# Optimization experiments

Hardware: AMD Instinct MI355X
Metric: run time of the kernel (lower is better)

The kernel has to match this reference:

```python
import jax, jax.numpy as jnp
import numpy as np

N = 1536          # num nodes
E = 49152         # num edges (avg degree 32)
D_IN = 32         # in_channels_node
D_EA = 2          # in_channels_edge_attr
D_ET = 2          # in_channels_edge_type
EMB = 32          # edge_attr_emb = edge_type_emb = node_emb = out_channels
HEADS = 3
SLOPE = 0.2


def leaky(x):
    return jax.nn.leaky_relu(x, negative_slope=SLOPE)


def setup_inputs() -> dict:
    key = jax.random.key(0)
    ks = jax.random.split(key, 12)
    node_f = jax.random.normal(ks[0], (N, D_IN), dtype=jnp.float32)
    edge_index = jax.random.randint(ks[1], (2, E), 0, N, dtype=jnp.int32)
    edge_attr = jax.random.normal(ks[2], (E, D_EA), dtype=jnp.float32)
    edge_type = jax.random.uniform(ks[3], (E, D_ET), dtype=jnp.float32)
    veh_node_mask = jax.random.bernoulli(ks[4], 0.7, (N,))
    ped_node_mask = jnp.logical_not(veh_node_mask)
    s = 0.1
    W_veh = jax.random.normal(ks[5], (EMB, D_IN), dtype=jnp.float32) * s
    W_ped = jax.random.normal(ks[6], (EMB, D_IN), dtype=jnp.float32) * s
    W_ea = jax.random.normal(ks[7], (EMB, D_EA), dtype=jnp.float32) * s
    W_et = jax.random.normal(ks[8], (EMB, D_ET), dtype=jnp.float32) * s
    # attention_nn: Linear(edge_attr_emb + edge_type_emb + 2*node_emb -> heads)
    W_att = jax.random.normal(ks[9], (HEADS, 2 * EMB + 2 * EMB), dtype=jnp.float32) * s
    # node_update_emb: Linear(edge_attr_emb + node_emb -> out_channels)
    W_upd = jax.random.normal(ks[10], (EMB, 2 * EMB), dtype=jnp.float32) * s
    return dict(node_f=node_f, edge_attr=edge_attr, edge_type=edge_type,
                W_veh=W_veh, W_ped=W_ped, W_ea=W_ea, W_et=W_et,
                W_att=W_att, W_upd=W_upd,
                edge_index=edge_index, veh_node_mask=veh_node_mask,
                ped_node_mask=ped_node_mask)


def reference(node_f, edge_attr, edge_type, W_veh, W_ped, W_ea, W_et,
              W_att, W_upd, edge_index, veh_node_mask, ped_node_mask):
    n = node_f.shape[0]
    src, dst = edge_index[0], edge_index[1]

    # edge embeddings [E, 32] each
    emb_ea = leaky(edge_attr @ W_ea.T)
    emb_et = leaky(edge_type.astype(node_f.dtype) @ W_et.T)
    edge_f = jnp.concatenate([emb_ea, emb_et], axis=-1)        # [E, 64]

    # densify (sparse_coo_tensor -> to_dense sums duplicate indices)
    dense_edge = jnp.zeros((n, n, 2 * EMB), node_f.dtype).at[src, dst].add(edge_f)
    dense_ea = jnp.zeros((n, n, EMB), node_f.dtype).at[src, dst].add(emb_ea)
    adj = jnp.zeros((n, n), node_f.dtype).at[src, dst].add(1.0)

    # type-specific node embedding (ped assignment last, matching torch overwrite order)
    node_emb = jnp.where(veh_node_mask[:, None], node_f @ W_veh.T, 0.0)
    node_emb = jnp.where(ped_node_mask[:, None], node_f @ W_ped.T, node_emb)
    node_emb = leaky(node_emb)                                  # [N, 32]

    # attention scores: split the linear over the concatenated [tar | edge | nbr] features
    W_tar, W_edge, W_nbr = W_att[:, :EMB], W_att[:, EMB:3 * EMB], W_att[:, 3 * EMB:]
    scores = leaky((node_emb @ W_tar.T)[:, None, :]
                   + jnp.einsum('ijc,hc->ijh', dense_edge, W_edge)
                   + (node_emb @ W_nbr.T)[None, :, :])          # [N, N, H]

    scores = jnp.where(adj[:, :, None] == 0.0, jnp.float32(-10000.0), scores)
    attn = jax.nn.softmax(scores, axis=1)                       # softmax over neighbors

    # node update features: Linear over [edge_attr_emb | nbr_emb]; identical across heads
    Wu_e, Wu_n = W_upd[:, :EMB], W_upd[:, EMB:]
    upd = leaky(jnp.einsum('ijc,oc->ijo', dense_ea, Wu_e)
                + (node_emb @ Wu_n.T)[None, :, :])              # [N, N, 32]

    # weighted aggregation over neighbors, then concat heads
    next_node_f = jnp.einsum('ijh,ijo->iho', attn, upd)         # [N, H, 32]
    return next_node_f.reshape(n, HEADS * EMB)
```

## Files before the change

### kernel.cpp

```cpp
#include <hip/hip_runtime.h>
#include <stdint.h>

#define NN 1536
#define EE 49152
#define EMB 32
#define HEADS 3
#define SLOPE 0.2f
#define CAP 72
#define EBLK (EE/256)
#define NBLK (NN/8)

__device__ __forceinline__ float lrelu(float x){ return x >= 0.f ? x : SLOPE*x; }

__device__ int detect_mask_layout(const unsigned char* p){
  const int* pi = (const int*)p;
  bool ok = true;
  for (int k=0;k<64 && ok;k++){ int v = pi[k]; ok = (v==0 || v==1); }
  if (ok) return 0;
  ok = true;
  for (int k=0;k<256 && ok;k++){ ok = (p[k] <= 1); }
  if (ok) return 1;
  return 2;
}
__device__ bool mask_at(const unsigned char* p, int layout, int i){
  if (layout==0) return ((const int*)p)[i] != 0;
  if (layout==1) return p[i] != 0;
  return ((const float*)p)[i] != 0.f;
}

__global__ __launch_bounds__(256) void k_prep(
    const float* __restrict__ node_f,
    const float* __restrict__ edge_attr, const float* __restrict__ edge_type,
    const float* __restrict__ W_veh, const float* __restrict__ W_ped,
    const float* __restrict__ W_att, const float* __restrict__ W_upd,
    const int* __restrict__ ei, const unsigned char* __restrict__ veh_mask,
    int* __restrict__ cnt, int* __restrict__ bucketD, float4* __restrict__ bucketF,
    float* __restrict__ tar, float* __restrict__ nbr, float* __restrict__ nb)
{
  const int t = threadIdx.x;
  const int b = blockIdx.x;

  if (b < EBLK){
    const int e = b*256 + t;
    const int s = ei[e], d = ei[EE + e];
    const float2 ea = ((const float2*)edge_attr)[e];
    const float2 et = ((const float2*)edge_type)[e];
    const int idx = atomicAdd(&cnt[s], 1);
    if (idx < CAP){
      bucketD[(size_t)s*CAP + idx] = d;
      bucketF[(size_t)s*CAP + idx] = make_float4(ea.x, ea.y, et.x, et.y);
    }
    return;
  }

  __shared__ float sWvehT[EMB*33], sWpedT[EMB*33], sWunT[EMB*33];
  __shared__ float sWt[HEADS*EMB], sWn[HEADS*EMB];
  __shared__ float sF[8*EMB], sEmb[8*EMB];
  __shared__ int layout_s;
  const int i0 = (b - EBLK)*8;
  if (t == 0) layout_s = detect_mask_layout(veh_mask);
  for (int idx=t; idx<EMB*EMB; idx+=256){
    const int mm = idx>>5, kk = idx&31;
    sWvehT[mm*33+kk] = W_veh[idx];
    sWpedT[mm*33+kk] = W_ped[idx];
    sWunT[mm*33+kk]  = W_upd[mm*64 + EMB + kk];
  }
  if (t < HEADS*EMB){
    const int h = t>>5, c = t&31;
    sWt[t] = W_att[h*128 + c];
    sWn[t] = W_att[h*128 + 96 + c];
  }
  sF[t] = node_f[(size_t)i0*EMB + t];
  __syncthreads();

  const int li = t >> 5, m = t & 31;
  const int i = i0 + li;
  const bool veh = mask_at(veh_mask, layout_s, i);
  const float* WT = veh ? sWvehT : sWpedT;
  float a = 0.f;
  #pragma unroll
  for (int k=0;k<EMB;k++) a += sF[li*EMB+k] * WT[m*33+k];
  sEmb[li*EMB+m] = lrelu(a);
  __syncthreads();

  float bb = 0.f;
  #pragma unroll
  for (int k=0;k<EMB;k++) bb += sEmb[li*EMB+k] * sWunT[m*33+k];
  nb[(size_t)i*EMB + m] = bb;
  if (m < 3){
    float v = 0.f;
    #pragma unroll
    for (int k=0;k<EMB;k++) v += sEmb[li*EMB+k] * sWt[m*EMB+k];
    tar[i*4+m] = v;
  } else if (m < 6){
    const int h = m-3;
    float v = 0.f;
    #pragma unroll
    for (int k=0;k<EMB;k++) v += sEmb[li*EMB+k] * sWn[h*EMB+k];
    nbr[i*4+h] = v;
  }
}

__global__ __launch_bounds__(256) void k_rows(
    const int* __restrict__ cnt, const int* __restrict__ bucketD,
    const float4* __restrict__ bucketF,
    const float* __restrict__ W_ea, const float* __restrict__ W_et,
    const float* __restrict__ W_att, const float* __restrict__ W_upd,
    const float* __restrict__ tar, const float* __restrict__ nbr,
    const float* __restrict__ nb, float* __restrict__ out)
{
  const int r = blockIdx.x;
  const int t = threadIdx.x;

  __shared__ int   ld[CAP], canon[CAP], slotidx[CAP], slotof[CAP], cdst[CAP];
  __shared__ float4 pay[CAP];
  __shared__ float sE[CAP*66];
  __shared__ float sWea[64], sWet[64], sWedge[HEADS*64], sWueT[EMB*33];
  __shared__ float pp[HEADS*CAP];
  __shared__ float partial[8*96];
  __shared__ float hden[HEADS];
  __shared__ int np_s;

  if (t < 64){ sWea[t] = W_ea[t]; sWet[t] = W_et[t]; }
  if (t < HEADS*64) sWedge[t] = W_att[(t>>6)*128 + EMB + (t&63)];
  for (int idx=t; idx<EMB*EMB; idx+=256){
    const int o = idx>>5, k = idx&31;
    sWueT[o*33+k] = W_upd[o*64 + k];
  }
  if (t == 0) np_s = 0;

  const int K = min(cnt[r], CAP);

  if (K == 0){
    __shared__ float fb[EMB];
    if (t < EMB) fb[t] = 0.f;
    __syncthreads();
    for (int idx=t; idx<NN*EMB; idx+=256) atomicAdd(&fb[idx&31], lrelu(nb[idx]));
    __syncthreads();
    if (t < 96) out[(size_t)r*96 + t] = fb[t&31] * (1.0f/NN);
    return;
  }

  for (int i=t; i<K; i+=256){
    ld[i]  = bucketD[(size_t)r*CAP + i];
    pay[i] = bucketF[(size_t)r*CAP + i];
    canon[i] = i;
  }
  __syncthreads();

  for (int p=t; p<K*K; p+=256){
    const int i = p / K, j = p - i*K;
    if (j < i && ld[i] == ld[j]) atomicMin(&canon[i], j);
  }
  __syncthreads();
  for (int i=t; i<K; i+=256){
    if (canon[i] == i){
      const int s2 = atomicAdd(&np_s, 1);
      slotidx[i] = s2;
      cdst[s2]   = ld[i];
    }
  }
  __syncthreads();
  const int Kc = np_s;
  const bool nodup = (Kc == K);

  for (int i=t; i<K; i+=256) slotof[i] = slotidx[canon[i]];
  if (!nodup){
    for (int idx=t; idx<Kc*66; idx+=256) sE[idx] = 0.f;
  }
  __syncthreads();

  for (int idx=t; idx<K*EMB; idx+=256){
    const int q = idx>>5, m = idx&31;
    const float4 p4 = pay[q];
    const float ea_ = lrelu(p4.x*sWea[2*m] + p4.y*sWea[2*m+1]);
    const float et_ = lrelu(p4.z*sWet[2*m] + p4.w*sWet[2*m+1]);
    const int sl = slotof[q];
    if (nodup){
      sE[sl*66 + m]      = ea_;
      sE[sl*66 + 33 + m] = et_;
    } else {
      atomicAdd(&sE[sl*66 + m],      ea_);
      atomicAdd(&sE[sl*66 + 33 + m], et_);
    }
  }
  __syncthreads();

  if (t < 192){
    const int h = t >> 6, lane = t & 63;
    const float th = tar[r*4+h];
    float mx = -1e30f;
    for (int q0=0; q0<Kc; q0+=64){
      const int q = q0 + lane;
      if (q < Kc){
        float sev = 0.f;
        #pragma unroll
        for (int k=0;k<EMB;k++)
          sev += sWedge[h*64+k]*sE[q*66+k] + sWedge[h*64+EMB+k]*sE[q*66+33+k];
        const float s = lrelu(th + sev + nbr[cdst[q]*4+h]);
        pp[h*CAP+q] = s;
        mx = fmaxf(mx, s);
      }
    }
    #pragma unroll
    for (int d=32; d; d>>=1) mx = fmaxf(mx, __shfl_xor(mx, d, 64));
    float den = 0.f;
    for (int q0=0; q0<Kc; q0+=64){
      const int q = q0 + lane;
      if (q < Kc){
        const float p = __expf(pp[h*CAP+q] - mx);
        pp[h*CAP+q] = p;
        den += p;
      }
    }
    #pragma unroll
    for (int d=32; d; d>>=1) den += __shfl_xor(den, d, 64);
    if (lane == 0) hden[h] = den;
  }
  __syncthreads();

  {
    const int g = t >> 5, o = t & 31;
    float a0=0.f, a1=0.f, a2=0.f;
    for (int q=g; q<Kc; q+=8){
      float ev = 0.f;
      #pragma unroll
      for (int k=0;k<EMB;k++) ev += sWueT[o*33+k] * sE[q*66+k];
      const float u = lrelu(ev + nb[(size_t)cdst[q]*EMB + o]);
      a0 += pp[0*CAP+q]*u;
      a1 += pp[1*CAP+q]*u;
      a2 += pp[2*CAP+q]*u;
    }
    partial[g*96 +      o] = a0;
    partial[g*96 + 32 + o] = a1;
    partial[g*96 + 64 + o] = a2;
  }
  __syncthreads();
  if (t < 96){
    float s = 0.f;
    #pragma unroll
    for (int g=0; g<8; g++) s += partial[g*96 + t];
    out[(size_t)r*96 + t] = s / hden[t>>5];
  }
}

extern "C" void kernel_launch(void* const* d_in, const int* in_sizes, int n_in,
                              void* d_out, int out_size, void* d_ws, size_t ws_size,
                              hipStream_t stream)
{
  (void)in_sizes; (void)n_in; (void)out_size; (void)ws_size;
  const float* node_f    = (const float*)d_in[0];
  const float* edge_attr = (const float*)d_in[1];
  const float* edge_type = (const float*)d_in[2];
  const float* W_veh     = (const float*)d_in[3];
  const float* W_ped     = (const float*)d_in[4];
  const float* W_ea      = (const float*)d_in[5];
  const float* W_et      = (const float*)d_in[6];
  const float* W_att     = (const float*)d_in[7];
  const float* W_upd     = (const float*)d_in[8];
  const int*   ei        = (const int*)d_in[9];
  const unsigned char* veh_mask = (const unsigned char*)d_in[10];
  float* out = (float*)d_out;

  char* ws = (char*)d_ws;
  const size_t oCnt  = 0;
  const size_t oBktF = oCnt  + (size_t)NN*4;
  const size_t oBktD = oBktF + (size_t)NN*CAP*16;
  const size_t oTar  = oBktD + (size_t)NN*CAP*4;
  const size_t oNbr  = oTar  + (size_t)NN*4*4;
  const size_t oNb   = oNbr  + (size_t)NN*4*4;

  int*    cnt     = (int*)   (ws + oCnt);
  float4* bucketF = (float4*)(ws + oBktF);
  int*    bucketD = (int*)   (ws + oBktD);
  float*  tar     = (float*) (ws + oTar);
  float*  nbr     = (float*) (ws + oNbr);
  float*  nb      = (float*) (ws + oNb);

  hipMemsetAsync(ws + oCnt, 0, (size_t)NN*4, stream);

  k_prep<<<EBLK + NBLK, 256, 0, stream>>>(node_f, edge_attr, edge_type,
                                          W_veh, W_ped, W_att, W_upd,
                                          ei, veh_mask, cnt, bucketD, bucketF,
                                          tar, nbr, nb);
  k_rows<<<NN, 256, 0, stream>>>(cnt, bucketD, bucketF, W_ea, W_et, W_att, W_upd,
                                 tar, nbr, nb, out);
}
```

Baseline: 117.0 us.

## Fuse prep and row kernels into one persistent kernel with grid barrier

Merges the bucketing/node-embedding kernel and the per-row attention kernel into a single launch of 768 blocks. Each block buckets 64 edges and embeds 2 nodes, then waits at a global atomic-counter barrier before processing 2 rows. Shared memory is unioned between the phases, and the target scores stay in shared memory instead of going through global memory. This removes a kernel launch boundary and the tail between the two launches. In exchange it relies on all 768 blocks being co-resident (launch bounds 256,3), adds a spin-wait barrier with a timeout, and gives each block two serial rows.

```diff
diff --git a/kernel.cpp b/kernel.cpp
--- a/kernel.cpp
+++ b/kernel.cpp
@@ -7,8 +7,7 @@
 #define HEADS 3
 #define SLOPE 0.2f
 #define CAP 72
-#define EBLK (EE/256)
-#define NBLK (NN/8)
+#define GRID 768
 
 __device__ __forceinline__ float lrelu(float x){ return x >= 0.f ? x : SLOPE*x; }
 
@@ -28,20 +27,77 @@
   return ((const float*)p)[i] != 0.f;
 }
 
-__global__ __launch_bounds__(256) void k_prep(
+#define O_PAY    0
+#define O_SE     1152
+#define O_PP     20160
+#define O_PART   21024
+#define O_LD     24096
+#define O_CANON  24384
+#define O_SLOTI  24672
+#define O_SLOTOF 24960
+#define O_CDST   25248
+#define UNI_SZ   25536
+#define A_VEH    0
+#define A_PED    4224
+#define A_UN     8448
+#define A_WT     12672
+#define A_WN     13056
+#define A_F      13440
+#define A_EMB    13696
+
+__global__ __launch_bounds__(256, 3) void k_fused(
     const float* __restrict__ node_f,
     const float* __restrict__ edge_attr, const float* __restrict__ edge_type,
     const float* __restrict__ W_veh, const float* __restrict__ W_ped,
+    const float* __restrict__ W_ea,  const float* __restrict__ W_et,
     const float* __restrict__ W_att, const float* __restrict__ W_upd,
     const int* __restrict__ ei, const unsigned char* __restrict__ veh_mask,
-    int* __restrict__ cnt, int* __restrict__ bucketD, float4* __restrict__ bucketF,
-    float* __restrict__ tar, float* __restrict__ nbr, float* __restrict__ nb)
+    int* __restrict__ cnt, int* done,
+    int* __restrict__ bucketD, float4* __restrict__ bucketF,
+    float* __restrict__ nbr, float* __restrict__ nb, float* __restrict__ out)
 {
   const int t = threadIdx.x;
   const int b = blockIdx.x;
 
-  if (b < EBLK){
-    const int e = b*256 + t;
+  __shared__ __align__(16) char uni[UNI_SZ];
+  __shared__ float sWea[64], sWet[64], sWedge[HEADS*64], sWueT[EMB*33];
+  __shared__ float tarL[2][4];
+  __shared__ float hden[HEADS];
+  __shared__ int np_s;
+  __shared__ int layout_s;
+
+  if (t < 64){ sWea[t] = W_ea[t]; sWet[t] = W_et[t]; }
+  if (t < HEADS*64) sWedge[t] = W_att[(t>>6)*128 + EMB + (t&63)];
+  for (int idx=t; idx<EMB*EMB; idx+=256){
+    const int o = idx>>5, k = idx&31;
+    sWueT[o*33+k] = W_upd[o*64 + k];
+  }
+  if (t == 0) layout_s = detect_mask_layout(veh_mask);
+
+  float* sWvehT = (float*)(uni + A_VEH);
+  float* sWpedT = (float*)(uni + A_PED);
+  float* sWunT  = (float*)(uni + A_UN);
+  float* sWt    = (float*)(uni + A_WT);
+  float* sWn    = (float*)(uni + A_WN);
+  float* sF     = (float*)(uni + A_F);
+  float* sEmb   = (float*)(uni + A_EMB);
+
+  for (int idx=t; idx<EMB*EMB; idx+=256){
+    const int mm = idx>>5, kk = idx&31;
+    sWvehT[mm*33+kk] = W_veh[idx];
+    sWpedT[mm*33+kk] = W_ped[idx];
+    sWunT[mm*33+kk]  = W_upd[mm*64 + EMB + kk];
+  }
+  if (t < HEADS*EMB){
+    const int h = t>>5, c = t&31;
+    sWt[t] = W_att[h*128 + c];
+    sWn[t] = W_att[h*128 + 96 + c];
+  }
+  if (t < 2*EMB) sF[t] = node_f[(size_t)(b*2)*EMB + t];
+  __syncthreads();
+
+  if (t < 64){
+    const int e = b*64 + t;
     const int s = ei[e], d = ei[EE + e];
     const float2 ea = ((const float2*)edge_attr)[e];
     const float2 et = ((const float2*)edge_type)[e];
@@ -50,197 +106,180 @@
       bucketD[(size_t)s*CAP + idx] = d;
       bucketF[(size_t)s*CAP + idx] = make_float4(ea.x, ea.y, et.x, et.y);
     }
-    return;
-  }
-
-  __shared__ float sWvehT[EMB*33], sWpedT[EMB*33], sWunT[EMB*33];
-  __shared__ float sWt[HEADS*EMB], sWn[HEADS*EMB];
-  __shared__ float sF[8*EMB], sEmb[8*EMB];
-  __shared__ int layout_s;
-  const int i0 = (b - EBLK)*8;
-  if (t == 0) layout_s = detect_mask_layout(veh_mask);
-  for (int idx=t; idx<EMB*EMB; idx+=256){
-    const int mm = idx>>5, kk = idx&31;
-    sWvehT[mm*33+kk] = W_veh[idx];
-    sWpedT[mm*33+kk] = W_ped[idx];
-    sWunT[mm*33+kk]  = W_upd[mm*64 + EMB + kk];
-  }
-  if (t < HEADS*EMB){
-    const int h = t>>5, c = t&31;
-    sWt[t] = W_att[h*128 + c];
-    sWn[t] = W_att[h*128 + 96 + c];
-  }
-  sF[t] = node_f[(size_t)i0*EMB + t];
+  } else if (t < 128){
+    const int li = (t-64) >> 5, m = t & 31;
+    const int i = b*2 + li;
+    const bool veh = mask_at(veh_mask, layout_s, i);
+    const float* WT = veh ? sWvehT : sWpedT;
+    float a = 0.f;
+    #pragma unroll
+    for (int k=0;k<EMB;k++) a += sF[li*EMB+k] * WT[m*33+k];
+    sEmb[li*EMB+m] = lrelu(a);
+  }
   __syncthreads();
 
-  const int li = t >> 5, m = t & 31;
-  const int i = i0 + li;
-  const bool veh = mask_at(veh_mask, layout_s, i);
-  const float* WT = veh ? sWvehT : sWpedT;
-  float a = 0.f;
-  #pragma unroll
-  for (int k=0;k<EMB;k++) a += sF[li*EMB+k] * WT[m*33+k];
-  sEmb[li*EMB+m] = lrelu(a);
+  if (t >= 64 && t < 128){
+    const int li = (t-64) >> 5, m = t & 31;
+    const int i = b*2 + li;
+    float bb = 0.f;
+    #pragma unroll
+    for (int k=0;k<EMB;k++) bb += sEmb[li*EMB+k] * sWunT[m*33+k];
+    nb[(size_t)i*EMB + m] = bb;
+    if (m < 3){
+      float v = 0.f;
+      #pragma unroll
+      for (int k=0;k<EMB;k++) v += sEmb[li*EMB+k] * sWt[m*EMB+k];
+      tarL[li][m] = v;
+    } else if (m < 6){
+      const int h = m-3;
+      float v = 0.f;
+      #pragma unroll
+      for (int k=0;k<EMB;k++) v += sEmb[li*EMB+k] * sWn[h*EMB+k];
+      nbr[i*4+h] = v;
+    }
+  }
+
+  __threadfence();
   __syncthreads();
-
-  float bb = 0.f;
-  #pragma unroll
-  for (int k=0;k<EMB;k++) bb += sEmb[li*EMB+k] * sWunT[m*33+k];
-  nb[(size_t)i*EMB + m] = bb;
-  if (m < 3){
-    float v = 0.f;
-    #pragma unroll
-    for (int k=0;k<EMB;k++) v += sEmb[li*EMB+k] * sWt[m*EMB+k];
-    tar[i*4+m] = v;
-  } else if (m < 6){
-    const int h = m-3;
-    float v = 0.f;
-    #pragma unroll
-    for (int k=0;k<EMB;k++) v += sEmb[li*EMB+k] * sWn[h*EMB+k];
-    nbr[i*4+h] = v;
-  }
-}
-
-__global__ __launch_bounds__(256) void k_rows(
-    const int* __restrict__ cnt, const int* __restrict__ bucketD,
-    const float4* __restrict__ bucketF,
-    const float* __restrict__ W_ea, const float* __restrict__ W_et,
-    const float* __restrict__ W_att, const float* __restrict__ W_upd,
-    const float* __restrict__ tar, const float* __restrict__ nbr,
-    const float* __restrict__ nb, float* __restrict__ out)
-{
-  const int r = blockIdx.x;
-  const int t = threadIdx.x;
-
-  __shared__ int   ld[CAP], canon[CAP], slotidx[CAP], slotof[CAP], cdst[CAP];
-  __shared__ float4 pay[CAP];
-  __shared__ float sE[CAP*66];
-  __shared__ float sWea[64], sWet[64], sWedge[HEADS*64], sWueT[EMB*33];
-  __shared__ float pp[HEADS*CAP];
-  __shared__ float partial[8*96];
-  __shared__ float hden[HEADS];
-  __shared__ int np_s;
-
-  if (t < 64){ sWea[t] = W_ea[t]; sWet[t] = W_et[t]; }
-  if (t < HEADS*64) sWedge[t] = W_att[(t>>6)*128 + EMB + (t&63)];
-  for (int idx=t; idx<EMB*EMB; idx+=256){
-    const int o = idx>>5, k = idx&31;
-    sWueT[o*33+k] = W_upd[o*64 + k];
-  }
-  if (t == 0) np_s = 0;
-
-  const int K = min(cnt[r], CAP);
-
-  if (K == 0){
-    __shared__ float fb[EMB];
-    if (t < EMB) fb[t] = 0.f;
-    __syncthreads();
-    for (int idx=t; idx<NN*EMB; idx+=256) atomicAdd(&fb[idx&31], lrelu(nb[idx]));
-    __syncthreads();
-    if (t < 96) out[(size_t)r*96 + t] = fb[t&31] * (1.0f/NN);
-    return;
-  }
-
-  for (int i=t; i<K; i+=256){
-    ld[i]  = bucketD[(size_t)r*CAP + i];
-    pay[i] = bucketF[(size_t)r*CAP + i];
-    canon[i] = i;
+  if (t == 0){
+    atomicAdd(done, 1);
+    int spins = 0;
+    while (atomicAdd(done, 0) < GRID){
+      __builtin_amdgcn_s_sleep(8);
+      if (++spins > 50000000) break;
+    }
   }
   __syncthreads();
-
-  for (int p=t; p<K*K; p+=256){
-    const int i = p / K, j = p - i*K;
-    if (j < i && ld[i] == ld[j]) atomicMin(&canon[i], j);
-  }
-  __syncthreads();
-  for (int i=t; i<K; i+=256){
-    if (canon[i] == i){
-      const int s2 = atomicAdd(&np_s, 1);
-      slotidx[i] = s2;
-      cdst[s2]   = ld[i];
-    }
-  }
-  __syncthreads();
-  const int Kc = np_s;
-  const bool nodup = (Kc == K);
-
-  for (int i=t; i<K; i+=256) slotof[i] = slotidx[canon[i]];
-  if (!nodup){
-    for (int idx=t; idx<Kc*66; idx+=256) sE[idx] = 0.f;
-  }
-  __syncthreads();
-
-  for (int idx=t; idx<K*EMB; idx+=256){
-    const int q = idx>>5, m = idx&31;
-    const float4 p4 = pay[q];
-    const float ea_ = lrelu(p4.x*sWea[2*m] + p4.y*sWea[2*m+1]);
-    const float et_ = lrelu(p4.z*sWet[2*m] + p4.w*sWet[2*m+1]);
-    const int sl = slotof[q];
-    if (nodup){
-      sE[sl*66 + m]      = ea_;
-      sE[sl*66 + 33 + m] = et_;
-    } else {
-      atomicAdd(&sE[sl*66 + m],      ea_);
-      atomicAdd(&sE[sl*66 + 33 + m], et_);
-    }
-  }
-  __syncthreads();
-
-  if (t < 192){
-    const int h = t >> 6, lane = t & 63;
-    const float th = tar[r*4+h];
-    float mx = -1e30f;
-    for (int q0=0; q0<Kc; q0+=64){
-      const int q = q0 + lane;
-      if (q < Kc){
-        float sev = 0.f;
+  __threadfence();
+
+  int*    ld      = (int*)   (uni + O_LD);
+  int*    canon   = (int*)   (uni + O_CANON);
+  int*    slotidx = (int*)   (uni + O_SLOTI);
+  int*    slotof  = (int*)   (uni + O_SLOTOF);
+  int*    cdst    = (int*)   (uni + O_CDST);
+  float4* pay     = (float4*)(uni + O_PAY);
+  float*  sE      = (float*) (uni + O_SE);
+  float*  pp      = (float*) (uni + O_PP);
+  float*  partial = (float*) (uni + O_PART);
+
+  for (int rr=0; rr<2; rr++){
+    const int r = b*2 + rr;
+    __syncthreads();
+    if (t == 0) np_s = 0;
+
+    const int K = min(cnt[r], CAP);
+
+    if (K == 0){
+      float* fb = (float*)(uni + O_PP);
+      if (t < EMB) fb[t] = 0.f;
+      __syncthreads();
+      for (int idx=t; idx<NN*EMB; idx+=256) atomicAdd(&fb[idx&31], lrelu(nb[idx]));
+      __syncthreads();
+      if (t < 96) out[(size_t)r*96 + t] = fb[t&31] * (1.0f/NN);
+      continue;
+    }
+
+    for (int i=t; i<K; i+=256){
+      ld[i]  = bucketD[(size_t)r*CAP + i];
+      pay[i] = bucketF[(size_t)r*CAP + i];
+      canon[i] = i;
+    }
+    __syncthreads();
+
+    for (int p=t; p<K*K; p+=256){
+      const int i = p / K, j = p - i*K;
+      if (j < i && ld[i] == ld[j]) atomicMin(&canon[i], j);
+    }
+    __syncthreads();
+    for (int i=t; i<K; i+=256){
+      if (canon[i] == i){
+        const int s2 = atomicAdd(&np_s, 1);
+        slotidx[i] = s2;
+        cdst[s2]   = ld[i];
+      }
+    }
+    __syncthreads();
+    const int Kc = np_s;
+    const bool nodup = (Kc == K);
+
+    for (int i=t; i<K; i+=256) slotof[i] = slotidx[canon[i]];
+    if (!nodup){
+      for (int idx=t; idx<Kc*66; idx+=256) sE[idx] = 0.f;
+    }
+    __syncthreads();
+
+    for (int idx=t; idx<K*EMB; idx+=256){
+      const int q = idx>>5, m = idx&31;
+      const float4 p4 = pay[q];
+      const float ea_ = lrelu(p4.x*sWea[2*m] + p4.y*sWea[2*m+1]);
+      const float et_ = lrelu(p4.z*sWet[2*m] + p4.w*sWet[2*m+1]);
+      const int sl = slotof[q];
+      if (nodup){
+        sE[sl*66 + m]      = ea_;
+        sE[sl*66 + 33 + m] = et_;
+      } else {
+        atomicAdd(&sE[sl*66 + m],      ea_);
+        atomicAdd(&sE[sl*66 + 33 + m], et_);
+      }
+    }
+    __syncthreads();
+
+    if (t < 192){
+      const int h = t >> 6, lane = t & 63;
+      const float th = tarL[rr][h];
+      float mx = -1e30f;
+      for (int q0=0; q0<Kc; q0+=64){
+        const int q = q0 + lane;
+        if (q < Kc){
+          float sev = 0.f;
+          #pragma unroll
+          for (int k=0;k<EMB;k++)
+            sev += sWedge[h*64+k]*sE[q*66+k] + sWedge[h*64+EMB+k]*sE[q*66+33+k];
+          const float s = lrelu(th + sev + nbr[cdst[q]*4+h]);
+          pp[h*CAP+q] = s;
+          mx = fmaxf(mx, s);
+        }
+      }
+      #pragma unroll
+      for (int d=32; d; d>>=1) mx = fmaxf(mx, __shfl_xor(mx, d, 64));
+      float den = 0.f;
+      for (int q0=0; q0<Kc; q0+=64){
+        const int q = q0 + lane;
+        if (q < Kc){
+          const float p = __expf(pp[h*CAP+q] - mx);
+          pp[h*CAP+q] = p;
+          den += p;
+        }
+      }
+      #pragma unroll
+      for (int d=32; d; d>>=1) den += __shfl_xor(den, d, 64);
+      if (lane == 0) hden[h] = den;
+    }
+    __syncthreads();
+
+    {
+      const int g = t >> 5, o = t & 31;
+      float a0=0.f, a1=0.f, a2=0.f;
+      for (int q=g; q<Kc; q+=8){
+        float ev = 0.f;
         #pragma unroll
-        for (int k=0;k<EMB;k++)
-          sev += sWedge[h*64+k]*sE[q*66+k] + sWedge[h*64+EMB+k]*sE[q*66+33+k];
-        const float s = lrelu(th + sev + nbr[cdst[q]*4+h]);
-        pp[h*CAP+q] = s;
-        mx = fmaxf(mx, s);
-      }
-    }
-    #pragma unroll
-    for (int d=32; d; d>>=1) mx = fmaxf(mx, __shfl_xor(mx, d, 64));
-    float den = 0.f;
-    for (int q0=0; q0<Kc; q0+=64){
-      const int q = q0 + lane;
-      if (q < Kc){
-        const float p = __expf(pp[h*CAP+q] - mx);
-        pp[h*CAP+q] = p;
-        den += p;
-      }
-    }
-    #pragma unroll
-    for (int d=32; d; d>>=1) den += __shfl_xor(den, d, 64);
-    if (lane == 0) hden[h] = den;
-  }
-  __syncthreads();
-
-  {
-    const int g = t >> 5, o = t & 31;
-    float a0=0.f, a1=0.f, a2=0.f;
-    for (int q=g; q<Kc; q+=8){
-      float ev = 0.f;
-      #pragma unroll
-      for (int k=0;k<EMB;k++) ev += sWueT[o*33+k] * sE[q*66+k];
-      const float u = lrelu(ev + nb[(size_t)cdst[q]*EMB + o]);
-      a0 += pp[0*CAP+q]*u;
-      a1 += pp[1*CAP+q]*u;
-      a2 += pp[2*CAP+q]*u;
-    }
-    partial[g*96 +      o] = a0;
-    partial[g*96 + 32 + o] = a1;
-    partial[g*96 + 64 + o] = a2;
-  }
-  __syncthreads();
-  if (t < 96){
-    float s = 0.f;
-    #pragma unroll
-    for (int g=0; g<8; g++) s += partial[g*96 + t];
-    out[(size_t)r*96 + t] = s / hden[t>>5];
+        for (int k=0;k<EMB;k++) ev += sWueT[o*33+k] * sE[q*66+k];
+        const float u = lrelu(ev + nb[(size_t)cdst[q]*EMB + o]);
+        a0 += pp[0*CAP+q]*u;
+        a1 += pp[1*CAP+q]*u;
+        a2 += pp[2*CAP+q]*u;
+      }
+      partial[g*96 +      o] = a0;
+      partial[g*96 + 32 + o] = a1;
+      partial[g*96 + 64 + o] = a2;
+    }
+    __syncthreads();
+    if (t < 96){
+      float s = 0.f;
+      #pragma unroll
+      for (int g=0; g<8; g++) s += partial[g*96 + t];
+      out[(size_t)r*96 + t] = s / hden[t>>5];
+    }
   }
 }
 
@@ -264,25 +303,23 @@
 
   char* ws = (char*)d_ws;
   const size_t oCnt  = 0;
-  const size_t oBktF = oCnt  + (size_t)NN*4;
+  const size_t oDone = (size_t)NN*4;
+  const size_t oBktF = oDone + 16;
   const size_t oBktD = oBktF + (size_t)NN*CAP*16;
-  const size_t oTar  = oBktD + (size_t)NN*CAP*4;
-  const size_t oNbr  = oTar  + (size_t)NN*4*4;
+  const size_t oNbr  = oBktD + (size_t)NN*CAP*4;
   const size_t oNb   = oNbr  + (size_t)NN*4*4;
 
   int*    cnt     = (int*)   (ws + oCnt);
+  int*    done    = (int*)   (ws + oDone);
   float4* bucketF = (float4*)(ws + oBktF);
   int*    bucketD = (int*)   (ws + oBktD);
-  float*  tar     = (float*) (ws + oTar);
   float*  nbr     = (float*) (ws + oNbr);
   float*  nb      = (float*) (ws + oNb);
 
-  hipMemsetAsync(ws + oCnt, 0, (size_t)NN*4, stream);
-
-  k_prep<<<EBLK + NBLK, 256, 0, stream>>>(node_f, edge_attr, edge_type,
-                                          W_veh, W_ped, W_att, W_upd,
-                                          ei, veh_mask, cnt, bucketD, bucketF,
-                                          tar, nbr, nb);
-  k_rows<<<NN, 256, 0, stream>>>(cnt, bucketD, bucketF, W_ea, W_et, W_att, W_upd,
-                                 tar, nbr, nb, out);
+  hipMemsetAsync(ws, 0, oBktF, stream);
+
+  k_fused<<<GRID, 256, 0, stream>>>(node_f, edge_attr, edge_type,
+                                    W_veh, W_ped, W_ea, W_et, W_att, W_upd,
+                                    ei, veh_mask, cnt, done, bucketD, bucketF,
+                                    nbr, nb, out);
 }
```

Result: slower. 277.3 us (+137.0%).

## Cut LDS use and barriers in row kernel, keep W_upd in registers

Applied to the files above, without the earlier changes.

The per-row kernel drops the shared transposed W_upd tile and instead loads each thread's W_upd row into eight float4 registers, reusing the pp buffer as fallback scratch. It also skips the dedup compaction pass and one barrier when a row has no duplicate destinations. It reduces the partial-sum buffer by folding wave halves with a shuffle, and changes the sE row stride to 67. A launch-bounds occupancy hint of 6 blocks is added. Together these aim to lower LDS footprint and sync overhead so more blocks fit per CU, at the cost of more register pressure.

```diff
diff --git a/kernel.cpp b/kernel.cpp
--- a/kernel.cpp
+++ b/kernel.cpp
@@ -7,6 +7,7 @@
 #define HEADS 3
 #define SLOPE 0.2f
 #define CAP 72
+#define SES 67
 #define EBLK (EE/256)
 #define NBLK (NN/8)
 
@@ -101,7 +102,7 @@
   }
 }
 
-__global__ __launch_bounds__(256) void k_rows(
+__global__ __launch_bounds__(256, 6) void k_rows(
     const int* __restrict__ cnt, const int* __restrict__ bucketD,
     const float4* __restrict__ bucketF,
     const float* __restrict__ W_ea, const float* __restrict__ W_et,
@@ -114,25 +115,21 @@
 
   __shared__ int   ld[CAP], canon[CAP], slotidx[CAP], slotof[CAP], cdst[CAP];
   __shared__ float4 pay[CAP];
-  __shared__ float sE[CAP*66];
-  __shared__ float sWea[64], sWet[64], sWedge[HEADS*64], sWueT[EMB*33];
+  __shared__ float sE[CAP*SES];
+  __shared__ float sWea[64], sWet[64], sWedge[HEADS*64];
   __shared__ float pp[HEADS*CAP];
-  __shared__ float partial[8*96];
+  __shared__ float partial[4*96];
   __shared__ float hden[HEADS];
-  __shared__ int np_s;
+  __shared__ int np_s, hasdup_s;
 
   if (t < 64){ sWea[t] = W_ea[t]; sWet[t] = W_et[t]; }
   if (t < HEADS*64) sWedge[t] = W_att[(t>>6)*128 + EMB + (t&63)];
-  for (int idx=t; idx<EMB*EMB; idx+=256){
-    const int o = idx>>5, k = idx&31;
-    sWueT[o*33+k] = W_upd[o*64 + k];
-  }
-  if (t == 0) np_s = 0;
+  if (t == 0){ np_s = 0; hasdup_s = 0; }
 
   const int K = min(cnt[r], CAP);
 
   if (K == 0){
-    __shared__ float fb[EMB];
+    float* fb = pp;
     if (t < EMB) fb[t] = 0.f;
     __syncthreads();
     for (int idx=t; idx<NN*EMB; idx+=256) atomicAdd(&fb[idx&31], lrelu(nb[idx]));
@@ -142,7 +139,9 @@
   }
 
   for (int i=t; i<K; i+=256){
-    ld[i]  = bucketD[(size_t)r*CAP + i];
+    const int d = bucketD[(size_t)r*CAP + i];
+    ld[i]  = d;
+    cdst[i] = d;
     pay[i] = bucketF[(size_t)r*CAP + i];
     canon[i] = i;
   }
@@ -150,38 +149,39 @@
 
   for (int p=t; p<K*K; p+=256){
     const int i = p / K, j = p - i*K;
-    if (j < i && ld[i] == ld[j]) atomicMin(&canon[i], j);
-  }
-  __syncthreads();
-  for (int i=t; i<K; i+=256){
-    if (canon[i] == i){
-      const int s2 = atomicAdd(&np_s, 1);
-      slotidx[i] = s2;
-      cdst[s2]   = ld[i];
-    }
-  }
-  __syncthreads();
-  const int Kc = np_s;
-  const bool nodup = (Kc == K);
-
-  for (int i=t; i<K; i+=256) slotof[i] = slotidx[canon[i]];
-  if (!nodup){
-    for (int idx=t; idx<Kc*66; idx+=256) sE[idx] = 0.f;
-  }
-  __syncthreads();
+    if (j < i && ld[i] == ld[j]){ atomicMin(&canon[i], j); hasdup_s = 1; }
+  }
+  __syncthreads();
+
+  const bool dup = (hasdup_s != 0);
+  int Kc = K;
+  if (dup){
+    for (int i=t; i<K; i+=256){
+      if (canon[i] == i){
+        const int s2 = atomicAdd(&np_s, 1);
+        slotidx[i] = s2;
+        cdst[s2]   = ld[i];
+      }
+    }
+    __syncthreads();
+    Kc = np_s;
+    for (int i=t; i<K; i+=256) slotof[i] = slotidx[canon[i]];
+    for (int idx=t; idx<Kc*SES; idx+=256) sE[idx] = 0.f;
+    __syncthreads();
+  }
 
   for (int idx=t; idx<K*EMB; idx+=256){
     const int q = idx>>5, m = idx&31;
     const float4 p4 = pay[q];
     const float ea_ = lrelu(p4.x*sWea[2*m] + p4.y*sWea[2*m+1]);
     const float et_ = lrelu(p4.z*sWet[2*m] + p4.w*sWet[2*m+1]);
-    const int sl = slotof[q];
-    if (nodup){
-      sE[sl*66 + m]      = ea_;
-      sE[sl*66 + 33 + m] = et_;
+    if (!dup){
+      sE[q*SES + m]      = ea_;
+      sE[q*SES + 33 + m] = et_;
     } else {
-      atomicAdd(&sE[sl*66 + m],      ea_);
-      atomicAdd(&sE[sl*66 + 33 + m], et_);
+      const int sl = slotof[q];
+      atomicAdd(&sE[sl*SES + m],      ea_);
+      atomicAdd(&sE[sl*SES + 33 + m], et_);
     }
   }
   __syncthreads();
@@ -196,7 +196,7 @@
         float sev = 0.f;
         #pragma unroll
         for (int k=0;k<EMB;k++)
-          sev += sWedge[h*64+k]*sE[q*66+k] + sWedge[h*64+EMB+k]*sE[q*66+33+k];
+          sev += sWedge[h*64+k]*sE[q*SES+k] + sWedge[h*64+EMB+k]*sE[q*SES+33+k];
         const float s = lrelu(th + sev + nbr[cdst[q]*4+h]);
         pp[h*CAP+q] = s;
         mx = fmaxf(mx, s);
@@ -221,25 +221,41 @@
 
   {
     const int g = t >> 5, o = t & 31;
+    const float4* wrow = (const float4*)(W_upd + (size_t)o*64);
+    const float4 w0=wrow[0], w1=wrow[1], w2=wrow[2], w3=wrow[3],
+                 w4=wrow[4], w5=wrow[5], w6=wrow[6], w7=wrow[7];
     float a0=0.f, a1=0.f, a2=0.f;
     for (int q=g; q<Kc; q+=8){
-      float ev = 0.f;
-      #pragma unroll
-      for (int k=0;k<EMB;k++) ev += sWueT[o*33+k] * sE[q*66+k];
+      const float* se = &sE[q*SES];
+      float ev;
+      ev  = w0.x*se[0]  + w0.y*se[1]  + w0.z*se[2]  + w0.w*se[3];
+      ev += w1.x*se[4]  + w1.y*se[5]  + w1.z*se[6]  + w1.w*se[7];
+      ev += w2.x*se[8]  + w2.y*se[9]  + w2.z*se[10] + w2.w*se[11];
+      ev += w3.x*se[12] + w3.y*se[13] + w3.z*se[14] + w3.w*se[15];
+      ev += w4.x*se[16] + w4.y*se[17] + w4.z*se[18] + w4.w*se[19];
+      ev += w5.x*se[20] + w5.y*se[21] + w5.z*se[22] + w5.w*se[23];
+      ev += w6.x*se[24] + w6.y*se[25] + w6.z*se[26] + w6.w*se[27];
+      ev += w7.x*se[28] + w7.y*se[29] + w7.z*se[30] + w7.w*se[31];
       const float u = lrelu(ev + nb[(size_t)cdst[q]*EMB + o]);
       a0 += pp[0*CAP+q]*u;
       a1 += pp[1*CAP+q]*u;
       a2 += pp[2*CAP+q]*u;
     }
-    partial[g*96 +      o] = a0;
-    partial[g*96 + 32 + o] = a1;
-    partial[g*96 + 64 + o] = a2;
+    a0 += __shfl_down(a0, 32, 64);
+    a1 += __shfl_down(a1, 32, 64);
+    a2 += __shfl_down(a2, 32, 64);
+    if ((g & 1) == 0){
+      const int gg = g >> 1;
+      partial[gg*96 +      o] = a0;
+      partial[gg*96 + 32 + o] = a1;
+      partial[gg*96 + 64 + o] = a2;
+    }
   }
   __syncthreads();
   if (t < 96){
     float s = 0.f;
     #pragma unroll
-    for (int g=0; g<8; g++) s += partial[g*96 + t];
+    for (int g=0; g<4; g++) s += partial[g*96 + t];
     out[(size_t)r*96 + t] = s / hden[t>>5];
   }
 }
```

Measured after the change: 120.3 us. 2.9% more time.
